# Performance work log

Hardware: AMD Instinct MI355X
Metric: run time of the kernel (lower is better)

The kernel has to match this reference:

```python
import jax, jax.numpy as jnp
import numpy as np

NUM_NODES = 10000
IN_DIM = 128
GAT_UNITS = 64
K = 20  # min(20, num_nodes - 1)
NEG_SLOPE = 0.2


def setup_inputs() -> dict:
    key = jax.random.key(0)
    ks = jax.random.split(key, 10)
    s = lambda k, shape, scale: jax.random.normal(k, shape, jnp.float32) * scale
    return {
        "x": s(ks[0], (NUM_NODES, IN_DIM), 1.0),
        "emb": s(ks[1], (NUM_NODES, 16), 1.0),
        "W1": s(ks[2], (IN_DIM, 4, GAT_UNITS), 0.05),
        "a1_src": s(ks[3], (4, GAT_UNITS), 0.05),
        "a1_tgt": s(ks[4], (4, GAT_UNITS), 0.05),
        "b1": jnp.zeros((4 * GAT_UNITS,), jnp.float32),
        "W2": s(ks[5], (4 * GAT_UNITS, 1, GAT_UNITS), 0.05),
        "a2_src": s(ks[6], (1, GAT_UNITS), 0.05),
        "a2_tgt": s(ks[7], (1, GAT_UNITS), 0.05),
        "b2": jnp.zeros((GAT_UNITS,), jnp.float32),
    }


def _build_edges(emb):
    # top-k adjacency from cosine similarity of node embeddings
    norm = emb / jnp.linalg.norm(emb, axis=-1, keepdims=True)
    sim = norm @ norm.T                      # [N, N]
    _, idx = jax.lax.top_k(sim, K)           # [N, K]
    n = emb.shape[0]
    src = jnp.repeat(jnp.arange(n, dtype=jnp.int32), K)
    tgt = idx.reshape(-1).astype(jnp.int32)
    # append self loops (as in the original module)
    loop = jnp.arange(n, dtype=jnp.int32)
    src = jnp.concatenate([src, loop])
    tgt = jnp.concatenate([tgt, loop])
    return src, tgt                          # each [N*(K+1)]


def _gat(x, W, a_src, a_tgt, src, tgt, n):
    # x: [N, F]; W: [F, H, C]; a_*: [H, C]
    h = jnp.einsum("nf,fhc->nhc", x, W)      # [N, H, C]
    e_src = jnp.einsum("nhc,hc->nh", h, a_src)  # [N, H]
    e_tgt = jnp.einsum("nhc,hc->nh", h, a_tgt)  # [N, H]
    logits = jax.nn.leaky_relu(e_src[src] + e_tgt[tgt], NEG_SLOPE)  # [E, H]
    # segment softmax over each source node's neighborhood
    m = jax.ops.segment_max(logits, src, num_segments=n)
    ex = jnp.exp(logits - m[src])
    z = jax.ops.segment_sum(ex, src, num_segments=n)
    alpha = ex / z[src]                      # [E, H]
    msg = alpha[:, :, None] * h[tgt]         # [E, H, C]
    return jax.ops.segment_sum(msg, src, num_segments=n)  # [N, H, C]


def reference(x, emb, W1, a1_src, a1_tgt, b1, W2, a2_src, a2_tgt, b2):
    n = x.shape[0]
    src, tgt = _build_edges(emb)
    # GAT layer 1: 4 heads, concatenated
    h1 = _gat(x, W1, a1_src, a1_tgt, src, tgt, n)        # [N, 4, C]
    h1 = h1.reshape(n, -1) + b1                           # [N, 4C]
    h1 = jax.nn.relu(h1)                                  # (dropout: inference mode)
    # GAT layer 2: 1 head, no concat
    h2 = _gat(h1, W2, a2_src, a2_tgt, src, tgt, n)        # [N, 1, C]
    return h2[:, 0, :] + b2                               # [N, C]
```

## Files before the change

kernel.cpp:

```cpp
#include <hip/hip_runtime.h>
#include <math.h>


#define N_NODES 10000
#define EMB_D   16
#define IN_DIM  128
#define H1      4
#define CDIM    64
#define D1      256
#define K_TOP   20
#define NEIGH   21
#define SROWS   32
#define NTILES  313
#define JSPLIT  2
#define HALFT   160
#define CAPM    96
#define GUARD   0.016f

typedef __attribute__((ext_vector_type(8)))  short short8;
typedef __attribute__((ext_vector_type(16))) float f32x16;

__device__ __forceinline__ unsigned monokey(float v) {
  unsigned u = __float_as_uint(v);
  return (u & 0x80000000u) ? ~u : (u | 0x80000000u);
}
__device__ __forceinline__ float invmono(unsigned m) {
  unsigned u = (m & 0x80000000u) ? (m ^ 0x80000000u) : ~m;
  return __uint_as_float(u);
}
__device__ __forceinline__ unsigned short f32_to_bf16(float f) {
  unsigned u = __float_as_uint(f);
  unsigned r = 0x7FFFu + ((u >> 16) & 1u);
  return (unsigned short)((u + r) >> 16);
}

__device__ __forceinline__ float dot16q(float4 qa, float4 qb, float4 qc, float4 qd,
                                        float4 v0, float4 v1, float4 v2, float4 v3) {
  float a = 0.f;
  a = fmaf(qa.x, v0.x, a); a = fmaf(qa.y, v0.y, a);
  a = fmaf(qa.z, v0.z, a); a = fmaf(qa.w, v0.w, a);
  a = fmaf(qb.x, v1.x, a); a = fmaf(qb.y, v1.y, a);
  a = fmaf(qb.z, v1.z, a); a = fmaf(qb.w, v1.w, a);
  a = fmaf(qc.x, v2.x, a); a = fmaf(qc.y, v2.y, a);
  a = fmaf(qc.z, v2.z, a); a = fmaf(qc.w, v2.w, a);
  a = fmaf(qd.x, v3.x, a); a = fmaf(qd.y, v3.y, a);
  a = fmaf(qd.z, v3.z, a); a = fmaf(qd.w, v3.w, a);
  return a;
}

__global__ __launch_bounds__(256) void normalize_kernel(
    const float* __restrict__ emb, float* __restrict__ nrm,
    unsigned short* __restrict__ nrmh) {
  int i = blockIdx.x * 256 + threadIdx.x;
  if (i >= N_NODES) return;
  const float4* p = (const float4*)(emb + (size_t)i * EMB_D);
  float4 v[4];
  float ss = 0.f;
#pragma unroll
  for (int k = 0; k < 4; k++) {
    v[k] = p[k];
    ss = fmaf(v[k].x, v[k].x, ss);
    ss = fmaf(v[k].y, v[k].y, ss);
    ss = fmaf(v[k].z, v[k].z, ss);
    ss = fmaf(v[k].w, v[k].w, ss);
  }
  float nv = sqrtf(ss);
  float4* o = (float4*)(nrm + (size_t)i * EMB_D);
  ushort4* oh = (ushort4*)(nrmh + (size_t)i * EMB_D);
#pragma unroll
  for (int k = 0; k < 4; k++) {
    float4 t;
    t.x = v[k].x / nv; t.y = v[k].y / nv; t.z = v[k].z / nv; t.w = v[k].w / nv;
    o[k] = t;
    ushort4 h;
    h.x = f32_to_bf16(t.x); h.y = f32_to_bf16(t.y);
    h.z = f32_to_bf16(t.z); h.w = f32_to_bf16(t.w);
    oh[k] = h;
  }
}

__global__ __launch_bounds__(512) void sim_topk_part(
    const float* __restrict__ nrm, const unsigned short* __restrict__ nrmh,
    unsigned long long* __restrict__ pkeys) {
  __shared__ unsigned short s_qbf[SROWS * EMB_D];
  __shared__ float s_qf[SROWS * EMB_D];
  __shared__ __align__(16) char s_ovl[32768];
  float (*s_smax)[256] = (float(*)[256])s_ovl;
  unsigned long long (*s_ckey)[CAPM] = (unsigned long long(*)[CAPM])s_ovl;
  unsigned short (*s_cid)[CAPM] =
      (unsigned short(*)[CAPM])(s_ovl + 24576);
  __shared__ float s_thr[SROWS];
  __shared__ int s_cnt[SROWS];

  int tid = threadIdx.x;
  int w = tid >> 6, lane = tid & 63;
  int lo5 = lane & 31, hi = lane >> 5;
  int row0 = blockIdx.x * SROWS;
  int bh = blockIdx.y;
  int tbase = bh * HALFT;

  if (tid < SROWS * EMB_D) {
    int gi = row0 * EMB_D + tid;
    float v = (gi < N_NODES * EMB_D) ? nrm[gi] : 0.f;
    s_qf[tid] = v;
    s_qbf[tid] = f32_to_bf16(v);
  }
  if (tid < SROWS) s_cnt[tid] = 0;
  __syncthreads();

  short8 afrag = *(const short8*)&s_qbf[lo5 * EMB_D + hi * 8];
  const f32x16 zacc = (f32x16)0.0f;

  float rm[16];
#pragma unroll
  for (int r = 0; r < 16; r++) rm[r] = -INFINITY;

#pragma unroll
  for (int g = 0; g < 5; ++g) {
    int tb = tbase + g * 32 + w * 4;
    int nd[4];
    short8 bf[4];
#pragma unroll
    for (int u = 0; u < 4; u++) {
      nd[u] = (tb + u) * 32 + lo5;
      bf[u] = (short8)(short)0;
      if (nd[u] < N_NODES)
        bf[u] = *(const short8*)&nrmh[(size_t)nd[u] * EMB_D + hi * 8];
    }
#pragma unroll
    for (int u = 0; u < 4; u++) {
      f32x16 acc = __builtin_amdgcn_mfma_f32_32x32x16_bf16(afrag, bf[u], zacc, 0, 0, 0);
      if (nd[u] < N_NODES) {
#pragma unroll
        for (int r = 0; r < 16; r++) rm[r] = fmaxf(rm[r], acc[r]);
      }
    }
  }
#pragma unroll
  for (int r = 0; r < 16; r++) {
    int rl = (r & 3) + 8 * (r >> 2) + 4 * hi;
    s_smax[rl][w * 32 + lo5] = rm[r];
  }
  __syncthreads();

  for (int q = 0; q < 4; q++) {
    int row = w * 4 + q;
    float m01 = fmaxf(s_smax[row][lane], s_smax[row][64 + lane]);
    float m23 = fmaxf(s_smax[row][128 + lane], s_smax[row][192 + lane]);
    unsigned v = monokey(fmaxf(m01, m23));
#pragma unroll
    for (int k = 2; k <= 64; k <<= 1) {
#pragma unroll
      for (int j = k >> 1; j > 0; j >>= 1) {
        unsigned o = __shfl_xor(v, j);
        bool upper = (lane & j) != 0;
        bool ascend = (lane & k) == 0;
        unsigned mx = v > o ? v : o;
        unsigned mn = v > o ? o : v;
        v = (upper == ascend) ? mx : mn;
      }
    }
    unsigned t20 = __shfl(v, 44);
    if (lane == 0)
      s_thr[row] = (row0 + row < N_NODES) ? invmono(t20) - GUARD : INFINITY;
  }
  __syncthreads();

  float thr_r[16];
#pragma unroll
  for (int r = 0; r < 16; r++)
    thr_r[r] = s_thr[(r & 3) + 8 * (r >> 2) + 4 * hi];

#pragma unroll
  for (int g = 0; g < 5; ++g) {
    int tb = tbase + g * 32 + w * 4;
    int nd[4];
    short8 bf[4];
#pragma unroll
    for (int u = 0; u < 4; u++) {
      nd[u] = (tb + u) * 32 + lo5;
      bf[u] = (short8)(short)0;
      if (nd[u] < N_NODES)
        bf[u] = *(const short8*)&nrmh[(size_t)nd[u] * EMB_D + hi * 8];
    }
#pragma unroll
    for (int u = 0; u < 4; u++) {
      f32x16 acc = __builtin_amdgcn_mfma_f32_32x32x16_bf16(afrag, bf[u], zacc, 0, 0, 0);
      if (nd[u] < N_NODES) {
#pragma unroll
        for (int r = 0; r < 16; r++) {
          if (acc[r] >= thr_r[r]) {
            int rl = (r & 3) + 8 * (r >> 2) + 4 * hi;
            int slot = atomicAdd(&s_cnt[rl], 1);
            if (slot < CAPM) s_cid[rl][slot] = (unsigned short)nd[u];
          }
        }
      }
    }
  }
  __syncthreads();

  for (int q = 0; q < 4; q++) {
    int row = w * 4 + q;
    if (row0 + row >= N_NODES) continue;
    int M = s_cnt[row];
    if (M > CAPM) continue;
    const float4* qp = (const float4*)&s_qf[row * EMB_D];
    float4 qa = qp[0], qb = qp[1], qc = qp[2], qd = qp[3];
    for (int c = lane; c < M; c += 64) {
      int id = s_cid[row][c];
      const float4* pj = (const float4*)(nrm + (size_t)id * EMB_D);
      float sim = dot16q(qa, qb, qc, qd, pj[0], pj[1], pj[2], pj[3]);
      s_ckey[row][c] = ((unsigned long long)monokey(sim) << 32) |
                       (unsigned long long)(0xFFFFFFFFu - (unsigned)id);
    }
  }
  __syncthreads();

  for (int q = 0; q < 4; q++) {
    int row = w * 4 + q;
    int grow = row0 + row;
    if (grow >= N_NODES) continue;
    unsigned long long* outp = pkeys + ((size_t)grow * JSPLIT + bh) * K_TOP;
    int M = s_cnt[row];
    if (M <= 64) {
      unsigned long long key = (lane < M) ? s_ckey[row][lane] : 0ull;
#pragma unroll
      for (int k = 2; k <= 64; k <<= 1) {
#pragma unroll
        for (int j = k >> 1; j > 0; j >>= 1) {
          unsigned long long o = __shfl_xor(key, j);
          bool upper = (lane & j) != 0;
          bool ascend = (lane & k) == 0;
          unsigned long long mx = key > o ? key : o;
          unsigned long long mn = key > o ? o : key;
          key = (upper == ascend) ? mx : mn;
        }
      }
      if (lane >= 64 - K_TOP) outp[63 - lane] = key;
    } else if (M <= CAPM) {
      for (int c = lane; c < M; c += 64) {
        unsigned long long mykey = s_ckey[row][c];
        int rank = 0;
        for (int i = 0; i < M; i++) rank += (s_ckey[row][i] > mykey) ? 1 : 0;
        if (rank < K_TOP) outp[rank] = mykey;
      }
    } else {
      const float4* qp = (const float4*)&s_qf[row * EMB_D];
      float4 qa = qp[0], qb = qp[1], qc = qp[2], qd = qp[3];
      int j0 = tbase * 32;
      int jend = j0 + HALFT * 32; if (jend > N_NODES) jend = N_NODES;
      unsigned long long prev = ~0ull;
      for (int r = 0; r < K_TOP; r++) {
        unsigned long long best = 0ull;
        for (int j = j0 + lane; j < jend; j += 64) {
          const float4* pj = (const float4*)(nrm + (size_t)j * EMB_D);
          float sim = dot16q(qa, qb, qc, qd, pj[0], pj[1], pj[2], pj[3]);
          unsigned long long key = ((unsigned long long)monokey(sim) << 32) |
                                   (unsigned long long)(0xFFFFFFFFu - (unsigned)j);
          if (key < prev && key > best) best = key;
        }
#pragma unroll
        for (int off = 32; off > 0; off >>= 1) {
          unsigned long long o = __shfl_down(best, off);
          if (o > best) best = o;
        }
        best = __shfl(best, 0);
        prev = best;
        if (lane == 0) outp[r] = best;
      }
    }
  }
}

__global__ __launch_bounds__(256) void topk_merge(
    const unsigned long long* __restrict__ pkeys, int* __restrict__ topk) {
  __shared__ unsigned long long s_k[4][JSPLIT * K_TOP];
  int w = threadIdx.x >> 6, lane = threadIdx.x & 63;
  int row = blockIdx.x * 4 + w;
  const unsigned long long* src = pkeys + (size_t)row * (JSPLIT * K_TOP);
  if (lane < JSPLIT * K_TOP) s_k[w][lane] = src[lane];
  __syncthreads();
  if (lane < JSPLIT * K_TOP) {
    unsigned long long mykey = s_k[w][lane];
    int rank = 0;
    for (int i = 0; i < JSPLIT * K_TOP; i++)
      rank += (s_k[w][i] > mykey) ? 1 : 0;
    if (rank < K_TOP)
      topk[(size_t)row * K_TOP + rank] =
          (int)(0xFFFFFFFFu - (unsigned)(mykey & 0xFFFFFFFFull));
  }
}

__global__ __launch_bounds__(256) void gemm1_kernel(
    const float* __restrict__ A, const float* __restrict__ B,
    const float* __restrict__ a_src, const float* __restrict__ a_tgt,
    float* __restrict__ Cc, float* __restrict__ es, float* __restrict__ et) {
  __shared__ float As[16][IN_DIM];
  int r0 = blockIdx.x * 16;
  int tid = threadIdx.x;
  {
    int rr = tid >> 4;
    int kk = tid & 15;
    ((float4*)&As[rr][0])[kk] = ((const float4*)(A + (size_t)(r0 + rr) * IN_DIM))[kk];
    ((float4*)&As[rr][0])[kk + 16] =
        ((const float4*)(A + (size_t)(r0 + rr) * IN_DIM))[kk + 16];
  }
  __syncthreads();
  int y = tid >> 7;
  int c0 = (tid & 127) * 2;
  float acc[8][2] = {};
  for (int k4 = 0; k4 < IN_DIM / 4; k4++) {
    float4 a[8];
#pragma unroll
    for (int r = 0; r < 8; r++) a[r] = ((const float4*)&As[y * 8 + r][0])[k4];
    float2 bv[4];
#pragma unroll
    for (int i = 0; i < 4; i++)
      bv[i] = *(const float2*)&B[(size_t)(k4 * 4 + i) * D1 + c0];
#pragma unroll
    for (int r = 0; r < 8; r++) {
      acc[r][0] = fmaf(a[r].x, bv[0].x, acc[r][0]);
      acc[r][1] = fmaf(a[r].x, bv[0].y, acc[r][1]);
      acc[r][0] = fmaf(a[r].y, bv[1].x, acc[r][0]);
      acc[r][1] = fmaf(a[r].y, bv[1].y, acc[r][1]);
      acc[r][0] = fmaf(a[r].z, bv[2].x, acc[r][0]);
      acc[r][1] = fmaf(a[r].z, bv[2].y, acc[r][1]);
      acc[r][0] = fmaf(a[r].w, bv[3].x, acc[r][0]);
      acc[r][1] = fmaf(a[r].w, bv[3].y, acc[r][1]);
    }
  }
#pragma unroll
  for (int r = 0; r < 8; r++) {
    float2 o = {acc[r][0], acc[r][1]};
    *(float2*)&Cc[(size_t)(r0 + y * 8 + r) * D1 + c0] = o;
  }
  int lane = tid & 63;
  int h = c0 >> 6;
  float as0 = a_src[c0], as1 = a_src[c0 + 1];
  float at0 = a_tgt[c0], at1 = a_tgt[c0 + 1];
#pragma unroll
  for (int r = 0; r < 8; r++) {
    float ps = fmaf(acc[r][1], as1, acc[r][0] * as0);
    float pt = fmaf(acc[r][1], at1, acc[r][0] * at0);
#pragma unroll
    for (int off = 16; off > 0; off >>= 1) {
      ps += __shfl_down(ps, off);
      pt += __shfl_down(pt, off);
    }
    if ((lane & 31) == 0) {
      es[(size_t)(r0 + y * 8 + r) * H1 + h] = ps;
      et[(size_t)(r0 + y * 8 + r) * H1 + h] = pt;
    }
  }
}

__global__ __launch_bounds__(256) void agg1_gemm2_kernel(
    const float* __restrict__ h1p, const float* __restrict__ e1s,
    const float* __restrict__ e1t, const int* __restrict__ topk,
    const float* __restrict__ b1, const float* __restrict__ B2,
    const float* __restrict__ a_src, const float* __restrict__ a_tgt,
    float* __restrict__ h2p, float* __restrict__ es, float* __restrict__ et) {
  __shared__ float As[16][D1];
  __shared__ int nb[16][NEIGH];
  __shared__ float wv[16][NEIGH][H1];
  __shared__ float zz[16][H1];
  int r0 = blockIdx.x * 16;
  int tid = threadIdx.x;

  for (int idx = tid; idx < 16 * NEIGH; idx += 256) {
    int n = idx / NEIGH, jj = idx % NEIGH;
    nb[n][jj] = (jj < K_TOP) ? topk[(size_t)(r0 + n) * K_TOP + jj] : (r0 + n);
  }
  __syncthreads();
  for (int idx = tid; idx < 16 * NEIGH * H1; idx += 256) {
    int e = idx & 3, jj = (idx >> 2) % NEIGH, n = idx / (NEIGH * H1);
    float L = e1s[(size_t)(r0 + n) * H1 + e] + e1t[(size_t)nb[n][jj] * H1 + e];
    wv[n][jj][e] = (L > 0.f) ? L : 0.2f * L;
  }
  __syncthreads();
  if (tid < 16 * H1) {
    int n = tid >> 2, h = tid & 3;
    float m = -INFINITY;
#pragma unroll
    for (int jj = 0; jj < NEIGH; jj++) m = fmaxf(m, wv[n][jj][h]);
    float z = 0.f;
#pragma unroll
    for (int jj = 0; jj < NEIGH; jj++) {
      float wt = expf(wv[n][jj][h] - m);
      z += wt;
      wv[n][jj][h] = wt;
    }
    zz[n][h] = z;
  }
  __syncthreads();
  {
    int h = tid >> 6;
    float bv = b1[tid];
    for (int n = 0; n < 16; n++) {
      float acc = 0.f;
#pragma unroll
      for (int jj = 0; jj < NEIGH; jj++)
        acc = fmaf(wv[n][jj][h], h1p[(size_t)nb[n][jj] * D1 + tid], acc);
      float o = acc / zz[n][h] + bv;
      As[n][tid] = fmaxf(o, 0.f);
    }
  }
  __syncthreads();
  int col = tid & 63, y = tid >> 6;
  float acc4[4] = {0, 0, 0, 0};
  for (int k4 = 0; k4 < D1 / 4; k4++) {
    float4 a[4];
#pragma unroll
    for (int r = 0; r < 4; r++) a[r] = ((const float4*)&As[y * 4 + r][0])[k4];
    float bv[4];
#pragma unroll
    for (int i = 0; i < 4; i++) bv[i] = B2[(size_t)(k4 * 4 + i) * CDIM + col];
#pragma unroll
    for (int r = 0; r < 4; r++) {
      acc4[r] = fmaf(a[r].x, bv[0], acc4[r]);
      acc4[r] = fmaf(a[r].y, bv[1], acc4[r]);
      acc4[r] = fmaf(a[r].z, bv[2], acc4[r]);
      acc4[r] = fmaf(a[r].w, bv[3], acc4[r]);
    }
  }
#pragma unroll
  for (int r = 0; r < 4; r++)
    h2p[(size_t)(r0 + y * 4 + r) * CDIM + col] = acc4[r];
  float as = a_src[col], at = a_tgt[col];
#pragma unroll
  for (int r = 0; r < 4; r++) {
    float ps = acc4[r] * as, pt = acc4[r] * at;
#pragma unroll
    for (int off = 32; off > 0; off >>= 1) {
      ps += __shfl_down(ps, off);
      pt += __shfl_down(pt, off);
    }
    if (col == 0) {
      es[r0 + y * 4 + r] = ps;
      et[r0 + y * 4 + r] = pt;
    }
  }
}

__global__ __launch_bounds__(256) void agg2_kernel(
    const float* __restrict__ h2p, const float* __restrict__ es,
    const float* __restrict__ et, const int* __restrict__ topk,
    const float* __restrict__ b2, float* __restrict__ out) {
  int tid = threadIdx.x;
  int li = tid >> 6;
  int c = tid & 63;
  int i = blockIdx.x * 4 + li;
  __shared__ int nb[4][NEIGH];
  __shared__ float lg[4][NEIGH];
  if (tid < 4 * NEIGH) {
    int li2 = tid / NEIGH, jj = tid % NEIGH;
    int node = blockIdx.x * 4 + li2;
    nb[li2][jj] = (jj < K_TOP) ? topk[(size_t)node * K_TOP + jj] : node;
  }
  __syncthreads();
  if (tid < 4 * NEIGH) {
    int li2 = tid / NEIGH, jj = tid % NEIGH;
    int node = blockIdx.x * 4 + li2;
    float L = es[node] + et[nb[li2][jj]];
    lg[li2][jj] = (L > 0.f) ? L : 0.2f * L;
  }
  __syncthreads();
  float m = -INFINITY;
#pragma unroll
  for (int jj = 0; jj < NEIGH; jj++) m = fmaxf(m, lg[li][jj]);
  float z = 0.f, acc = 0.f;
#pragma unroll
  for (int jj = 0; jj < NEIGH; jj++) {
    float w = expf(lg[li][jj] - m);
    z += w;
    acc = fmaf(w, h2p[(size_t)nb[li][jj] * CDIM + c], acc);
  }
  out[(size_t)i * CDIM + c] = acc / z + b2[c];
}

extern "C" void kernel_launch(void* const* d_in, const int* in_sizes, int n_in,
                              void* d_out, int out_size, void* d_ws, size_t ws_size,
                              hipStream_t stream) {
  const float* x   = (const float*)d_in[0];
  const float* emb = (const float*)d_in[1];
  const float* W1  = (const float*)d_in[2];
  const float* a1s = (const float*)d_in[3];
  const float* a1t = (const float*)d_in[4];
  const float* b1  = (const float*)d_in[5];
  const float* W2  = (const float*)d_in[6];
  const float* a2s = (const float*)d_in[7];
  const float* a2t = (const float*)d_in[8];
  const float* b2  = (const float*)d_in[9];
  float* out = (float*)d_out;

  size_t off = 0;
  auto alloc = [&](size_t bytes) {
    void* p = (char*)d_ws + off;
    off += (bytes + 255) & ~(size_t)255;
    return p;
  };
  float*          nrm  = (float*)alloc((size_t)N_NODES * EMB_D * sizeof(float));
  unsigned short* nrmh = (unsigned short*)alloc((size_t)N_NODES * EMB_D * sizeof(unsigned short));
  int*   topk = (int*)  alloc((size_t)N_NODES * K_TOP * sizeof(int));
  float* h1p  = (float*)alloc((size_t)N_NODES * D1 * sizeof(float));
  float* e1s  = (float*)alloc((size_t)N_NODES * H1 * sizeof(float));
  float* e1t  = (float*)alloc((size_t)N_NODES * H1 * sizeof(float));
  float* h2p  = (float*)alloc((size_t)N_NODES * CDIM * sizeof(float));
  float* e2s  = (float*)alloc((size_t)N_NODES * sizeof(float));
  float* e2t  = (float*)alloc((size_t)N_NODES * sizeof(float));
  unsigned long long* pkeys = (unsigned long long*)h1p;
  (void)ws_size; (void)in_sizes; (void)n_in; (void)out_size;

  normalize_kernel<<<(N_NODES + 255) / 256, 256, 0, stream>>>(emb, nrm, nrmh);
  sim_topk_part<<<dim3(NTILES, JSPLIT), 512, 0, stream>>>(nrm, nrmh, pkeys);
  topk_merge<<<N_NODES / 4, 256, 0, stream>>>(pkeys, topk);
  gemm1_kernel<<<N_NODES / 16, 256, 0, stream>>>(x, W1, a1s, a1t, h1p, e1s, e1t);
  agg1_gemm2_kernel<<<N_NODES / 16, 256, 0, stream>>>(h1p, e1s, e1t, topk, b1,
                                                      W2, a2s, a2t, h2p, e2s, e2t);
  agg2_kernel<<<N_NODES / 4, 256, 0, stream>>>(h2p, e2s, e2t, topk, b2, out);
}
```

Measured before the change: 144.1 us.

## Fuse similarity top-k partial kernel with layer-1 GEMM via block-index dispatch

Merges the similarity/top-k partial kernel and the first GAT projection GEMM into one launch, where the first blocks do the top-k work and the remaining blocks do the x·W1 GEMM with 32 rows per 512-thread block. The two independent stages can now run concurrently on the GPU and one launch is dropped. The partial-key buffer gets its own workspace allocation instead of aliasing h1p, which removes the write conflict this concurrency would otherwise cause. The bitonic-sort path for small candidate counts is also removed, so every row with up to CAPM candidates uses the rank-counting path.

```diff
diff --git a/kernel.cpp b/kernel.cpp
--- a/kernel.cpp
+++ b/kernel.cpp
@@ -16,6 +16,8 @@
 #define HALFT   160
 #define CAPM    96
 #define GUARD   0.016f
+#define SIMB    (NTILES * JSPLIT)
+#define G1B     313
 
 typedef __attribute__((ext_vector_type(8)))  short short8;
 typedef __attribute__((ext_vector_type(16))) float f32x16;
@@ -79,195 +81,247 @@
   }
 }
 
-__global__ __launch_bounds__(512) void sim_topk_part(
+__global__ __launch_bounds__(512) void sim_gemm1_fused(
     const float* __restrict__ nrm, const unsigned short* __restrict__ nrmh,
-    unsigned long long* __restrict__ pkeys) {
-  __shared__ unsigned short s_qbf[SROWS * EMB_D];
-  __shared__ float s_qf[SROWS * EMB_D];
-  __shared__ __align__(16) char s_ovl[32768];
-  float (*s_smax)[256] = (float(*)[256])s_ovl;
-  unsigned long long (*s_ckey)[CAPM] = (unsigned long long(*)[CAPM])s_ovl;
-  unsigned short (*s_cid)[CAPM] =
-      (unsigned short(*)[CAPM])(s_ovl + 24576);
-  __shared__ float s_thr[SROWS];
-  __shared__ int s_cnt[SROWS];
-
+    unsigned long long* __restrict__ pkeys,
+    const float* __restrict__ A, const float* __restrict__ B,
+    const float* __restrict__ a_src, const float* __restrict__ a_tgt,
+    float* __restrict__ Cc, float* __restrict__ es, float* __restrict__ et) {
+  __shared__ __align__(16) char smem[36096];
   int tid = threadIdx.x;
-  int w = tid >> 6, lane = tid & 63;
-  int lo5 = lane & 31, hi = lane >> 5;
-  int row0 = blockIdx.x * SROWS;
-  int bh = blockIdx.y;
-  int tbase = bh * HALFT;
-
-  if (tid < SROWS * EMB_D) {
-    int gi = row0 * EMB_D + tid;
-    float v = (gi < N_NODES * EMB_D) ? nrm[gi] : 0.f;
-    s_qf[tid] = v;
-    s_qbf[tid] = f32_to_bf16(v);
-  }
-  if (tid < SROWS) s_cnt[tid] = 0;
-  __syncthreads();
-
-  short8 afrag = *(const short8*)&s_qbf[lo5 * EMB_D + hi * 8];
-  const f32x16 zacc = (f32x16)0.0f;
-
-  float rm[16];
-#pragma unroll
-  for (int r = 0; r < 16; r++) rm[r] = -INFINITY;
-
-#pragma unroll
-  for (int g = 0; g < 5; ++g) {
-    int tb = tbase + g * 32 + w * 4;
-    int nd[4];
-    short8 bf[4];
-#pragma unroll
-    for (int u = 0; u < 4; u++) {
-      nd[u] = (tb + u) * 32 + lo5;
-      bf[u] = (short8)(short)0;
-      if (nd[u] < N_NODES)
-        bf[u] = *(const short8*)&nrmh[(size_t)nd[u] * EMB_D + hi * 8];
-    }
-#pragma unroll
-    for (int u = 0; u < 4; u++) {
-      f32x16 acc = __builtin_amdgcn_mfma_f32_32x32x16_bf16(afrag, bf[u], zacc, 0, 0, 0);
-      if (nd[u] < N_NODES) {
-#pragma unroll
-        for (int r = 0; r < 16; r++) rm[r] = fmaxf(rm[r], acc[r]);
-      }
-    }
-  }
-#pragma unroll
-  for (int r = 0; r < 16; r++) {
-    int rl = (r & 3) + 8 * (r >> 2) + 4 * hi;
-    s_smax[rl][w * 32 + lo5] = rm[r];
-  }
-  __syncthreads();
-
-  for (int q = 0; q < 4; q++) {
-    int row = w * 4 + q;
-    float m01 = fmaxf(s_smax[row][lane], s_smax[row][64 + lane]);
-    float m23 = fmaxf(s_smax[row][128 + lane], s_smax[row][192 + lane]);
-    unsigned v = monokey(fmaxf(m01, m23));
-#pragma unroll
-    for (int k = 2; k <= 64; k <<= 1) {
-#pragma unroll
-      for (int j = k >> 1; j > 0; j >>= 1) {
-        unsigned o = __shfl_xor(v, j);
-        bool upper = (lane & j) != 0;
-        bool ascend = (lane & k) == 0;
-        unsigned mx = v > o ? v : o;
-        unsigned mn = v > o ? o : v;
-        v = (upper == ascend) ? mx : mn;
-      }
-    }
-    unsigned t20 = __shfl(v, 44);
-    if (lane == 0)
-      s_thr[row] = (row0 + row < N_NODES) ? invmono(t20) - GUARD : INFINITY;
-  }
-  __syncthreads();
-
-  float thr_r[16];
-#pragma unroll
-  for (int r = 0; r < 16; r++)
-    thr_r[r] = s_thr[(r & 3) + 8 * (r >> 2) + 4 * hi];
-
-#pragma unroll
-  for (int g = 0; g < 5; ++g) {
-    int tb = tbase + g * 32 + w * 4;
-    int nd[4];
-    short8 bf[4];
-#pragma unroll
-    for (int u = 0; u < 4; u++) {
-      nd[u] = (tb + u) * 32 + lo5;
-      bf[u] = (short8)(short)0;
-      if (nd[u] < N_NODES)
-        bf[u] = *(const short8*)&nrmh[(size_t)nd[u] * EMB_D + hi * 8];
-    }
-#pragma unroll
-    for (int u = 0; u < 4; u++) {
-      f32x16 acc = __builtin_amdgcn_mfma_f32_32x32x16_bf16(afrag, bf[u], zacc, 0, 0, 0);
-      if (nd[u] < N_NODES) {
-#pragma unroll
-        for (int r = 0; r < 16; r++) {
-          if (acc[r] >= thr_r[r]) {
-            int rl = (r & 3) + 8 * (r >> 2) + 4 * hi;
-            int slot = atomicAdd(&s_cnt[rl], 1);
-            if (slot < CAPM) s_cid[rl][slot] = (unsigned short)nd[u];
+  int bid = blockIdx.x;
+
+  if (bid < SIMB) {
+    unsigned short* s_qbf = (unsigned short*)smem;
+    float* s_qf = (float*)(smem + 1024);
+    char* s_ovl = smem + 3072;
+    float (*s_smax)[256] = (float(*)[256])s_ovl;
+    unsigned long long (*s_ckey)[CAPM] = (unsigned long long(*)[CAPM])s_ovl;
+    unsigned short (*s_cid)[CAPM] = (unsigned short(*)[CAPM])(s_ovl + 24576);
+    float* s_thr = (float*)(smem + 35840);
+    int* s_cnt = (int*)(smem + 35968);
+
+    int w = tid >> 6, lane = tid & 63;
+    int lo5 = lane & 31, hi = lane >> 5;
+    int row0 = (bid >> 1) * SROWS;
+    int bh = bid & 1;
+    int tbase = bh * HALFT;
+
+    if (tid < SROWS * EMB_D) {
+      int gi = row0 * EMB_D + tid;
+      float v = (gi < N_NODES * EMB_D) ? nrm[gi] : 0.f;
+      s_qf[tid] = v;
+      s_qbf[tid] = f32_to_bf16(v);
+    }
+    if (tid < SROWS) s_cnt[tid] = 0;
+    __syncthreads();
+
+    short8 afrag = *(const short8*)&s_qbf[lo5 * EMB_D + hi * 8];
+    const f32x16 zacc = (f32x16)0.0f;
+
+    float rm[16];
+#pragma unroll
+    for (int r = 0; r < 16; r++) rm[r] = -INFINITY;
+#pragma unroll
+    for (int g = 0; g < 5; ++g) {
+      int tb = tbase + g * 32 + w * 4;
+      int nd[4];
+      short8 bf[4];
+#pragma unroll
+      for (int u = 0; u < 4; u++) {
+        nd[u] = (tb + u) * 32 + lo5;
+        bf[u] = (short8)(short)0;
+        if (nd[u] < N_NODES)
+          bf[u] = *(const short8*)&nrmh[(size_t)nd[u] * EMB_D + hi * 8];
+      }
+#pragma unroll
+      for (int u = 0; u < 4; u++) {
+        f32x16 acc = __builtin_amdgcn_mfma_f32_32x32x16_bf16(afrag, bf[u], zacc, 0, 0, 0);
+        if (nd[u] < N_NODES) {
+#pragma unroll
+          for (int r = 0; r < 16; r++) rm[r] = fmaxf(rm[r], acc[r]);
+        }
+      }
+    }
+#pragma unroll
+    for (int r = 0; r < 16; r++) {
+      int rl = (r & 3) + 8 * (r >> 2) + 4 * hi;
+      s_smax[rl][w * 32 + lo5] = rm[r];
+    }
+    __syncthreads();
+
+    for (int q = 0; q < 4; q++) {
+      int row = w * 4 + q;
+      float m01 = fmaxf(s_smax[row][lane], s_smax[row][64 + lane]);
+      float m23 = fmaxf(s_smax[row][128 + lane], s_smax[row][192 + lane]);
+      unsigned v = monokey(fmaxf(m01, m23));
+#pragma unroll
+      for (int k = 2; k <= 64; k <<= 1) {
+#pragma unroll
+        for (int j = k >> 1; j > 0; j >>= 1) {
+          unsigned o = __shfl_xor(v, j);
+          bool upper = (lane & j) != 0;
+          bool ascend = (lane & k) == 0;
+          unsigned mx = v > o ? v : o;
+          unsigned mn = v > o ? o : v;
+          v = (upper == ascend) ? mx : mn;
+        }
+      }
+      unsigned t20 = __shfl(v, 44);
+      if (lane == 0)
+        s_thr[row] = (row0 + row < N_NODES) ? invmono(t20) - GUARD : INFINITY;
+    }
+    __syncthreads();
+
+    float thr_r[16];
+#pragma unroll
+    for (int r = 0; r < 16; r++)
+      thr_r[r] = s_thr[(r & 3) + 8 * (r >> 2) + 4 * hi];
+
+#pragma unroll
+    for (int g = 0; g < 5; ++g) {
+      int tb = tbase + g * 32 + w * 4;
+      int nd[4];
+      short8 bf[4];
+#pragma unroll
+      for (int u = 0; u < 4; u++) {
+        nd[u] = (tb + u) * 32 + lo5;
+        bf[u] = (short8)(short)0;
+        if (nd[u] < N_NODES)
+          bf[u] = *(const short8*)&nrmh[(size_t)nd[u] * EMB_D + hi * 8];
+      }
+#pragma unroll
+      for (int u = 0; u < 4; u++) {
+        f32x16 acc = __builtin_amdgcn_mfma_f32_32x32x16_bf16(afrag, bf[u], zacc, 0, 0, 0);
+        if (nd[u] < N_NODES) {
+#pragma unroll
+          for (int r = 0; r < 16; r++) {
+            if (acc[r] >= thr_r[r]) {
+              int rl = (r & 3) + 8 * (r >> 2) + 4 * hi;
+              int slot = atomicAdd(&s_cnt[rl], 1);
+              if (slot < CAPM) s_cid[rl][slot] = (unsigned short)nd[u];
+            }
           }
         }
       }
     }
-  }
-  __syncthreads();
-
-  for (int q = 0; q < 4; q++) {
-    int row = w * 4 + q;
-    if (row0 + row >= N_NODES) continue;
-    int M = s_cnt[row];
-    if (M > CAPM) continue;
-    const float4* qp = (const float4*)&s_qf[row * EMB_D];
-    float4 qa = qp[0], qb = qp[1], qc = qp[2], qd = qp[3];
-    for (int c = lane; c < M; c += 64) {
-      int id = s_cid[row][c];
-      const float4* pj = (const float4*)(nrm + (size_t)id * EMB_D);
-      float sim = dot16q(qa, qb, qc, qd, pj[0], pj[1], pj[2], pj[3]);
-      s_ckey[row][c] = ((unsigned long long)monokey(sim) << 32) |
-                       (unsigned long long)(0xFFFFFFFFu - (unsigned)id);
-    }
-  }
-  __syncthreads();
-
-  for (int q = 0; q < 4; q++) {
-    int row = w * 4 + q;
-    int grow = row0 + row;
-    if (grow >= N_NODES) continue;
-    unsigned long long* outp = pkeys + ((size_t)grow * JSPLIT + bh) * K_TOP;
-    int M = s_cnt[row];
-    if (M <= 64) {
-      unsigned long long key = (lane < M) ? s_ckey[row][lane] : 0ull;
-#pragma unroll
-      for (int k = 2; k <= 64; k <<= 1) {
-#pragma unroll
-        for (int j = k >> 1; j > 0; j >>= 1) {
-          unsigned long long o = __shfl_xor(key, j);
-          bool upper = (lane & j) != 0;
-          bool ascend = (lane & k) == 0;
-          unsigned long long mx = key > o ? key : o;
-          unsigned long long mn = key > o ? o : key;
-          key = (upper == ascend) ? mx : mn;
-        }
-      }
-      if (lane >= 64 - K_TOP) outp[63 - lane] = key;
-    } else if (M <= CAPM) {
-      for (int c = lane; c < M; c += 64) {
-        unsigned long long mykey = s_ckey[row][c];
-        int rank = 0;
-        for (int i = 0; i < M; i++) rank += (s_ckey[row][i] > mykey) ? 1 : 0;
-        if (rank < K_TOP) outp[rank] = mykey;
-      }
-    } else {
+    __syncthreads();
+
+    for (int q = 0; q < 4; q++) {
+      int row = w * 4 + q;
+      if (row0 + row >= N_NODES) continue;
+      int M = s_cnt[row];
+      if (M > CAPM) continue;
       const float4* qp = (const float4*)&s_qf[row * EMB_D];
       float4 qa = qp[0], qb = qp[1], qc = qp[2], qd = qp[3];
-      int j0 = tbase * 32;
-      int jend = j0 + HALFT * 32; if (jend > N_NODES) jend = N_NODES;
-      unsigned long long prev = ~0ull;
-      for (int r = 0; r < K_TOP; r++) {
-        unsigned long long best = 0ull;
-        for (int j = j0 + lane; j < jend; j += 64) {
-          const float4* pj = (const float4*)(nrm + (size_t)j * EMB_D);
-          float sim = dot16q(qa, qb, qc, qd, pj[0], pj[1], pj[2], pj[3]);
-          unsigned long long key = ((unsigned long long)monokey(sim) << 32) |
-                                   (unsigned long long)(0xFFFFFFFFu - (unsigned)j);
-          if (key < prev && key > best) best = key;
+      for (int c = lane; c < M; c += 64) {
+        int id = s_cid[row][c];
+        const float4* pj = (const float4*)(nrm + (size_t)id * EMB_D);
+        float sim = dot16q(qa, qb, qc, qd, pj[0], pj[1], pj[2], pj[3]);
+        s_ckey[row][c] = ((unsigned long long)monokey(sim) << 32) |
+                         (unsigned long long)(0xFFFFFFFFu - (unsigned)id);
+      }
+    }
+    __syncthreads();
+
+    for (int q = 0; q < 4; q++) {
+      int row = w * 4 + q;
+      int grow = row0 + row;
+      if (grow >= N_NODES) continue;
+      unsigned long long* outp = pkeys + ((size_t)grow * JSPLIT + bh) * K_TOP;
+      int M = s_cnt[row];
+      if (M <= CAPM) {
+        for (int c = lane; c < M; c += 64) {
+          unsigned long long mykey = s_ckey[row][c];
+          int rank = 0;
+          for (int i = 0; i < M; i++) rank += (s_ckey[row][i] > mykey) ? 1 : 0;
+          if (rank < K_TOP) outp[rank] = mykey;
         }
-#pragma unroll
-        for (int off = 32; off > 0; off >>= 1) {
-          unsigned long long o = __shfl_down(best, off);
-          if (o > best) best = o;
+      } else {
+        const float4* qp = (const float4*)&s_qf[row * EMB_D];
+        float4 qa = qp[0], qb = qp[1], qc = qp[2], qd = qp[3];
+        int j0 = tbase * 32;
+        int jend = j0 + HALFT * 32; if (jend > N_NODES) jend = N_NODES;
+        unsigned long long prev = ~0ull;
+        for (int r = 0; r < K_TOP; r++) {
+          unsigned long long best = 0ull;
+          for (int j = j0 + lane; j < jend; j += 64) {
+            const float4* pj = (const float4*)(nrm + (size_t)j * EMB_D);
+            float sim = dot16q(qa, qb, qc, qd, pj[0], pj[1], pj[2], pj[3]);
+            unsigned long long key = ((unsigned long long)monokey(sim) << 32) |
+                                     (unsigned long long)(0xFFFFFFFFu - (unsigned)j);
+            if (key < prev && key > best) best = key;
+          }
+#pragma unroll
+          for (int off = 32; off > 0; off >>= 1) {
+            unsigned long long o = __shfl_down(best, off);
+            if (o > best) best = o;
+          }
+          best = __shfl(best, 0);
+          prev = best;
+          if (lane == 0) outp[r] = best;
         }
-        best = __shfl(best, 0);
-        prev = best;
-        if (lane == 0) outp[r] = best;
+      }
+    }
+  } else {
+    float (*As)[IN_DIM] = (float(*)[IN_DIM])smem;
+    int r0 = (bid - SIMB) * 32;
+    const float4 z4 = {0.f, 0.f, 0.f, 0.f};
+    for (int e = tid; e < 32 * (IN_DIM / 4); e += 512) {
+      int rr = e >> 5, kk = e & 31;
+      int row = r0 + rr;
+      ((float4*)&As[rr][0])[kk] =
+          (row < N_NODES) ? ((const float4*)(A + (size_t)row * IN_DIM))[kk] : z4;
+    }
+    __syncthreads();
+    int y = tid >> 7;
+    int c0 = (tid & 127) * 2;
+    float acc[8][2] = {};
+    for (int k4 = 0; k4 < IN_DIM / 4; k4++) {
+      float4 a[8];
+#pragma unroll
+      for (int r = 0; r < 8; r++) a[r] = ((const float4*)&As[y * 8 + r][0])[k4];
+      float2 bv[4];
+#pragma unroll
+      for (int i = 0; i < 4; i++)
+        bv[i] = *(const float2*)&B[(size_t)(k4 * 4 + i) * D1 + c0];
+#pragma unroll
+      for (int r = 0; r < 8; r++) {
+        acc[r][0] = fmaf(a[r].x, bv[0].x, acc[r][0]);
+        acc[r][1] = fmaf(a[r].x, bv[0].y, acc[r][1]);
+        acc[r][0] = fmaf(a[r].y, bv[1].x, acc[r][0]);
+        acc[r][1] = fmaf(a[r].y, bv[1].y, acc[r][1]);
+        acc[r][0] = fmaf(a[r].z, bv[2].x, acc[r][0]);
+        acc[r][1] = fmaf(a[r].z, bv[2].y, acc[r][1]);
+        acc[r][0] = fmaf(a[r].w, bv[3].x, acc[r][0]);
+        acc[r][1] = fmaf(a[r].w, bv[3].y, acc[r][1]);
+      }
+    }
+#pragma unroll
+    for (int r = 0; r < 8; r++) {
+      int row = r0 + y * 8 + r;
+      if (row < N_NODES) {
+        float2 o = {acc[r][0], acc[r][1]};
+        *(float2*)&Cc[(size_t)row * D1 + c0] = o;
+      }
+    }
+    int lane = tid & 63;
+    int h = c0 >> 6;
+    float as0 = a_src[c0], as1 = a_src[c0 + 1];
+    float at0 = a_tgt[c0], at1 = a_tgt[c0 + 1];
+#pragma unroll
+    for (int r = 0; r < 8; r++) {
+      float ps = fmaf(acc[r][1], as1, acc[r][0] * as0);
+      float pt = fmaf(acc[r][1], at1, acc[r][0] * at0);
+#pragma unroll
+      for (int off = 16; off > 0; off >>= 1) {
+        ps += __shfl_down(ps, off);
+        pt += __shfl_down(pt, off);
+      }
+      int row = r0 + y * 8 + r;
+      if ((lane & 31) == 0 && row < N_NODES) {
+        es[(size_t)row * H1 + h] = ps;
+        et[(size_t)row * H1 + h] = pt;
       }
     }
   }
@@ -289,69 +343,6 @@
     if (rank < K_TOP)
       topk[(size_t)row * K_TOP + rank] =
           (int)(0xFFFFFFFFu - (unsigned)(mykey & 0xFFFFFFFFull));
-  }
-}
-
-__global__ __launch_bounds__(256) void gemm1_kernel(
-    const float* __restrict__ A, const float* __restrict__ B,
-    const float* __restrict__ a_src, const float* __restrict__ a_tgt,
-    float* __restrict__ Cc, float* __restrict__ es, float* __restrict__ et) {
-  __shared__ float As[16][IN_DIM];
-  int r0 = blockIdx.x * 16;
-  int tid = threadIdx.x;
-  {
-    int rr = tid >> 4;
-    int kk = tid & 15;
-    ((float4*)&As[rr][0])[kk] = ((const float4*)(A + (size_t)(r0 + rr) * IN_DIM))[kk];
-    ((float4*)&As[rr][0])[kk + 16] =
-        ((const float4*)(A + (size_t)(r0 + rr) * IN_DIM))[kk + 16];
-  }
-  __syncthreads();
-  int y = tid >> 7;
-  int c0 = (tid & 127) * 2;
-  float acc[8][2] = {};
-  for (int k4 = 0; k4 < IN_DIM / 4; k4++) {
-    float4 a[8];
-#pragma unroll
-    for (int r = 0; r < 8; r++) a[r] = ((const float4*)&As[y * 8 + r][0])[k4];
-    float2 bv[4];
-#pragma unroll
-    for (int i = 0; i < 4; i++)
-      bv[i] = *(const float2*)&B[(size_t)(k4 * 4 + i) * D1 + c0];
-#pragma unroll
-    for (int r = 0; r < 8; r++) {
-      acc[r][0] = fmaf(a[r].x, bv[0].x, acc[r][0]);
-      acc[r][1] = fmaf(a[r].x, bv[0].y, acc[r][1]);
-      acc[r][0] = fmaf(a[r].y, bv[1].x, acc[r][0]);
-      acc[r][1] = fmaf(a[r].y, bv[1].y, acc[r][1]);
-      acc[r][0] = fmaf(a[r].z, bv[2].x, acc[r][0]);
-      acc[r][1] = fmaf(a[r].z, bv[2].y, acc[r][1]);
-      acc[r][0] = fmaf(a[r].w, bv[3].x, acc[r][0]);
-      acc[r][1] = fmaf(a[r].w, bv[3].y, acc[r][1]);
-    }
-  }
-#pragma unroll
-  for (int r = 0; r < 8; r++) {
-    float2 o = {acc[r][0], acc[r][1]};
-    *(float2*)&Cc[(size_t)(r0 + y * 8 + r) * D1 + c0] = o;
-  }
-  int lane = tid & 63;
-  int h = c0 >> 6;
-  float as0 = a_src[c0], as1 = a_src[c0 + 1];
-  float at0 = a_tgt[c0], at1 = a_tgt[c0 + 1];
-#pragma unroll
-  for (int r = 0; r < 8; r++) {
-    float ps = fmaf(acc[r][1], as1, acc[r][0] * as0);
-    float pt = fmaf(acc[r][1], at1, acc[r][0] * at0);
-#pragma unroll
-    for (int off = 16; off > 0; off >>= 1) {
-      ps += __shfl_down(ps, off);
-      pt += __shfl_down(pt, off);
-    }
-    if ((lane & 31) == 0) {
-      es[(size_t)(r0 + y * 8 + r) * H1 + h] = ps;
-      et[(size_t)(r0 + y * 8 + r) * H1 + h] = pt;
-    }
   }
 }
 
@@ -509,13 +500,14 @@
   float* h2p  = (float*)alloc((size_t)N_NODES * CDIM * sizeof(float));
   float* e2s  = (float*)alloc((size_t)N_NODES * sizeof(float));
   float* e2t  = (float*)alloc((size_t)N_NODES * sizeof(float));
-  unsigned long long* pkeys = (unsigned long long*)h1p;
+  unsigned long long* pkeys =
+      (unsigned long long*)alloc((size_t)N_NODES * JSPLIT * K_TOP * sizeof(unsigned long long));
   (void)ws_size; (void)in_sizes; (void)n_in; (void)out_size;
 
   normalize_kernel<<<(N_NODES + 255) / 256, 256, 0, stream>>>(emb, nrm, nrmh);
-  sim_topk_part<<<dim3(NTILES, JSPLIT), 512, 0, stream>>>(nrm, nrmh, pkeys);
+  sim_gemm1_fused<<<SIMB + G1B, 512, 0, stream>>>(nrm, nrmh, pkeys,
+                                                  x, W1, a1s, a1t, h1p, e1s, e1t);
   topk_merge<<<N_NODES / 4, 256, 0, stream>>>(pkeys, topk);
-  gemm1_kernel<<<N_NODES / 16, 256, 0, stream>>>(x, W1, a1s, a1t, h1p, e1s, e1t);
   agg1_gemm2_kernel<<<N_NODES / 16, 256, 0, stream>>>(h1p, e1s, e1t, topk, b1,
                                                       W2, a2s, a2t, h2p, e2s, e2t);
   agg2_kernel<<<N_NODES / 4, 256, 0, stream>>>(h2p, e2s, e2t, topk, b2, out);
```

Result: slower. 148.7 us (+3.1%).
